# Kernel optimization log

Hardware: AMD Instinct MI355X
Metric: run time of the kernel (lower is better)

Reference implementation:

```python
import jax, jax.numpy as jnp
import numpy as np

VOCAB = 100000
TOPK = 20
EMB = 300
BS, SEQ = 64, 256

def setup_inputs() -> dict:
    key = jax.random.key(0)
    k1, k2, k3, k4, k5 = jax.random.split(key, 5)
    conceptnet_text_vec = jax.random.randint(k1, (BS, SEQ), 0, VOCAB)
    neighbors = jax.random.randint(k2, (VOCAB, TOPK), 0, VOCAB)
    emb = jax.random.normal(k3, (VOCAB, EMB), dtype=jnp.float32)
    # xavier-normal init for attention params
    a = jax.random.normal(k4, (EMB, EMB), dtype=jnp.float32) * np.sqrt(2.0 / (EMB + EMB))
    b = jax.random.normal(k5, (EMB, 1), dtype=jnp.float32) * np.sqrt(2.0 / (EMB + 1))
    return {"conceptnet_text_vec": conceptnet_text_vec, "neighbors": neighbors,
            "emb": emb, "a": a, "b": b}

def reference(conceptnet_text_vec, neighbors, emb, a, b):
    # double gather: ids -> neighbor ids -> neighbor embeddings
    nb = neighbors[conceptnet_text_vec]          # [B, S, K] int
    h = emb[nb]                                  # [B, S, K, D]
    # tanh attention scores over the K (neighbor) dim
    e = jnp.einsum('bske,e->bsk', jnp.tanh(jnp.einsum('bskd,de->bske', h, a)), b[:, 0])
    att = jax.nn.softmax(e, axis=-1)             # [B, S, K]
    return jnp.einsum('bsk,bskd->bsd', att, h)   # [B, S, D]
```

## Files before the change

kernel.cpp:

```cpp
#include <hip/hip_runtime.h>
#include <hip/hip_bf16.h>
#include <math.h>

#define VOCAB 100000
#define TOPK  20
#define EMB   300
#define NTOK  (64*256)
#define NB    1563
#define NSLICE 128

typedef __attribute__((ext_vector_type(8))) short short8;
typedef __attribute__((ext_vector_type(4))) short short4v;
typedef __attribute__((ext_vector_type(4))) float f32x4;

static __device__ inline short f2bf(float f) {
    __hip_bfloat16 h = __float2bfloat16(f);
    short s; __builtin_memcpy(&s, &h, 2);
    return s;
}

__global__ void prep_kernel(const float* __restrict__ A, short* __restrict__ aT)
{
    const int e = blockIdx.x;
    for (int d = threadIdx.x; d < 320; d += 256) {
        float f = (e < EMB && d < EMB) ? A[(size_t)d * EMB + e] : 0.f;
        aT[e * 320 + d] = f2bf(f);
    }
}

__global__ __launch_bounds__(512, 2) void score_kernel(
    const float* __restrict__ emb, const short* __restrict__ aT,
    const float* __restrict__ B, float* __restrict__ S0, float* __restrict__ S1)
{
    __shared__ short8 BsS[160 * 40];
    __shared__ short8 EsS[64 * 40];
    __shared__ float  Sred[128];

    const int t     = threadIdx.x;
    const int eh    = blockIdx.x >> 7;
    const int slice = blockIdx.x & 127;

#pragma unroll
    for (int j = 0; j < 13; ++j) {
        const int i = t + j * 512;
        if (i < 6400) {
            const int col = i / 40, kc = i - col * 40;
            short8 v = ((const short8*)aT)[(eh * 160 + col) * 40 + kc];
            BsS[col * 40 + (kc ^ (col & 7))] = v;
        }
    }

    const int lid = t & 63;
    const int w   = t >> 6;
    const int kh  = w >> 2;
    const int mg  = (w >> 1) & 1;
    const int ng  = w & 1;
    const int lm  = lid & 15;
    const int lk  = lid >> 4;
    const int kh20  = kh * 20;
    const int xmask = lm & 7;

    int colb[5], rb[2];
    float bcol[5];
#pragma unroll
    for (int g = 0; g < 5; ++g) {
        const int col = (ng * 5 + g) * 16 + lm;
        colb[g] = col * 40;
        const int e = eh * 160 + col;
        bcol[g] = (e < EMB) ? B[e] : 0.f;
    }
#pragma unroll
    for (int mt = 0; mt < 2; ++mt)
        rb[mt] = (mg * 32 + mt * 16 + lm) * 40;

    const int ntiles = (NB - slice + NSLICE - 1) / NSLICE;
    float4 pf[10];

    {
        const float4* esrc = (const float4*)(emb + (size_t)slice * 64 * EMB);
#pragma unroll
        for (int j = 0; j < 10; ++j) {
            const int p4 = t + j * 512;
            float4 f = make_float4(0.f, 0.f, 0.f, 0.f);
            if (p4 < 4800 && slice * 64 + p4 / 75 < VOCAB) f = esrc[p4];
            pf[j] = f;
        }
    }

    for (int tt = 0; tt < ntiles; ++tt) {
        const int tile = slice + tt * NSLICE;
        const int v0   = tile * 64;

#pragma unroll
        for (int j = 0; j < 10; ++j) {
            const int p4 = t + j * 512;
            if (p4 < 4800) {
                const int row = p4 / 75, c4 = p4 - row * 75;
                short4v h;
                h.x = f2bf(pf[j].x); h.y = f2bf(pf[j].y);
                h.z = f2bf(pf[j].z); h.w = f2bf(pf[j].w);
                short* base = (short*)&EsS[row * 40 + ((c4 >> 1) ^ (row & 7))];
                *(short4v*)(base + (c4 & 1) * 4) = h;
            }
        }
        if (t < 320) {
            const int row = t / 5, q = t - row * 5;
            const int cc = 37 + ((q + 1) >> 1), half = (q + 1) & 1;
            short* base = (short*)&EsS[row * 40 + (cc ^ (row & 7))];
            *(short4v*)(base + half * 4) = (short4v){0, 0, 0, 0};
        }

        if (tt + 1 < ntiles) {
            const int tn = tile + NSLICE;
            const float4* esrc = (const float4*)(emb + (size_t)tn * 64 * EMB);
#pragma unroll
            for (int j = 0; j < 10; ++j) {
                const int p4 = t + j * 512;
                float4 f = make_float4(0.f, 0.f, 0.f, 0.f);
                if (p4 < 4800 && tn * 64 + p4 / 75 < VOCAB) f = esrc[p4];
                pf[j] = f;
            }
        }
        __syncthreads();

        f32x4 acc[2][5];
#pragma unroll
        for (int mt = 0; mt < 2; ++mt)
#pragma unroll
            for (int g = 0; g < 5; ++g)
                acc[mt][g] = (f32x4){0.f, 0.f, 0.f, 0.f};

        short8 bfr[2][5], afr[2][2];
        {
            const int kx = (kh20 + lk) ^ xmask;
#pragma unroll
            for (int g = 0; g < 5; ++g) bfr[0][g] = BsS[colb[g] + kx];
#pragma unroll
            for (int mt = 0; mt < 2; ++mt) afr[0][mt] = EsS[rb[mt] + kx];
        }
#pragma unroll
        for (int ks = 0; ks < 5; ++ks) {
            const int cur = ks & 1, nx = cur ^ 1;
            if (ks < 4) {
                const int kx = (kh20 + (ks + 1) * 4 + lk) ^ xmask;
#pragma unroll
                for (int g = 0; g < 5; ++g) bfr[nx][g] = BsS[colb[g] + kx];
#pragma unroll
                for (int mt = 0; mt < 2; ++mt) afr[nx][mt] = EsS[rb[mt] + kx];
            }
#pragma unroll
            for (int mt = 0; mt < 2; ++mt)
#pragma unroll
                for (int g = 0; g < 5; ++g)
                    acc[mt][g] = __builtin_amdgcn_mfma_f32_16x16x32_bf16(
                                     afr[cur][mt], bfr[cur][g], acc[mt][g], 0, 0, 0);
        }
        __syncthreads();

        float* scratchF = (float*)EsS;
        const int cell = mg * 2 + ng;
        if (kh == 1) {
#pragma unroll
            for (int mt = 0; mt < 2; ++mt)
#pragma unroll
                for (int g = 0; g < 5; ++g)
#pragma unroll
                    for (int i = 0; i < 4; ++i) {
                        const int q = (mt * 5 + g) * 4 + i;
                        scratchF[(q * 4 + cell) * 64 + lid] = acc[mt][g][i];
                    }
        }
        __syncthreads();

        if (kh == 0) {
            float part[2][4];
#pragma unroll
            for (int mt = 0; mt < 2; ++mt)
#pragma unroll
                for (int i = 0; i < 4; ++i) {
                    float p = 0.f;
#pragma unroll
                    for (int g = 0; g < 5; ++g) {
                        const int q = (mt * 5 + g) * 4 + i;
                        float x  = acc[mt][g][i] + scratchF[(q * 4 + cell) * 64 + lid];
                        float xc = fminf(fmaxf(x, -15.f), 15.f);
                        float e2 = __expf(2.f * xc);
                        p += __fdividef(e2 - 1.f, e2 + 1.f) * bcol[g];
                    }
                    part[mt][i] = p;
                }
#pragma unroll
            for (int m = 1; m <= 8; m <<= 1)
#pragma unroll
                for (int mt = 0; mt < 2; ++mt)
#pragma unroll
                    for (int i = 0; i < 4; ++i)
                        part[mt][i] += __shfl_xor(part[mt][i], m);
            if (lm == 0) {
#pragma unroll
                for (int mt = 0; mt < 2; ++mt)
#pragma unroll
                    for (int i = 0; i < 4; ++i)
                        Sred[ng * 64 + mg * 32 + mt * 16 + lk * 4 + i] = part[mt][i];
            }
        }
        __syncthreads();

        if (t < 64) {
            const int v = v0 + t;
            if (v < VOCAB) {
                float* Sp = eh ? S1 : S0;
                Sp[v] = Sred[t] + Sred[64 + t];
            }
        }
    }
}

__global__ __launch_bounds__(256) void attend_kernel(
    const int* __restrict__ text, const int* __restrict__ neighbors,
    const float* __restrict__ emb, const float* __restrict__ S0,
    const float* __restrict__ S1, float* __restrict__ out)
{
    const int lane = threadIdx.x & 63;
    const int wv   = threadIdx.x >> 6;
    const int tok  = blockIdx.x * 4 + wv;

    const int tid = text[tok];

    int   nbk = 0;
    float sc  = -1e30f;
    if (lane < TOPK) {
        nbk = neighbors[tid * TOPK + lane];
        sc  = S0[nbk] + S1[nbk];
    }

    float mx = sc;
#pragma unroll
    for (int m = 16; m >= 1; m >>= 1)
        mx = fmaxf(mx, __shfl_xor(mx, m));

    float ex = (lane < TOPK) ? expf(sc - mx) : 0.f;
    float sum = ex;
#pragma unroll
    for (int m = 16; m >= 1; m >>= 1)
        sum += __shfl_xor(sum, m);
    float att = ex / sum;

    float acc0 = 0.f, acc1 = 0.f, acc2 = 0.f, acc3 = 0.f, acc4 = 0.f;
    const bool has5 = (lane < EMB - 256);
#pragma unroll 4
    for (int k = 0; k < TOPK; ++k) {
        const float wgt = __shfl(att, k);
        const int   id  = __shfl(nbk, k);
        const float* row = emb + (size_t)id * EMB;
        acc0 = fmaf(wgt, row[lane      ], acc0);
        acc1 = fmaf(wgt, row[lane +  64], acc1);
        acc2 = fmaf(wgt, row[lane + 128], acc2);
        acc3 = fmaf(wgt, row[lane + 192], acc3);
        if (has5) acc4 = fmaf(wgt, row[lane + 256], acc4);
    }

    float* orow = out + (size_t)tok * EMB;
    orow[lane      ] = acc0;
    orow[lane +  64] = acc1;
    orow[lane + 128] = acc2;
    orow[lane + 192] = acc3;
    if (has5) orow[lane + 256] = acc4;
}

extern "C" void kernel_launch(void* const* d_in, const int* in_sizes, int n_in,
                              void* d_out, int out_size, void* d_ws, size_t ws_size,
                              hipStream_t stream) {
    const int*   text      = (const int*)d_in[0];
    const int*   neighbors = (const int*)d_in[1];
    const float* emb       = (const float*)d_in[2];
    const float* A         = (const float*)d_in[3];
    const float* B         = (const float*)d_in[4];
    float*       out       = (float*)d_out;

    char* ws = (char*)d_ws;
    float* S0 = (float*)ws;
    float* S1 = (float*)(ws + 400000);
    short* aT = (short*)(ws + 800000);

    prep_kernel<<<320, 256, 0, stream>>>(A, aT);
    score_kernel<<<256, 512, 0, stream>>>(emb, aT, B, S0, S1);
    attend_kernel<<<NTOK / 4, 256, 0, stream>>>(text, neighbors, emb, S0, S1, out);
}
```

Before: 129.0 us.

## Hold A-matrix fragments in registers and split tanh epilogue across both K-halves

The score kernel now loads each wave's bf16 A-transpose fragments straight into registers once, so the shared-memory B tile and its per-k-step LDS reads go away. The split-K reduction is rebalanced: each K-half writes the partial of the other's M-tile into a dedicated float4 scratch buffer, and both halves run the tanh/score epilogue, where before only one half did. Staging of the next embedding tile is moved into the reduction phase, and the emb loads use 8-element chunks with a separate tail load. This increases register pressure (25 short8 fragments held per thread) under the existing 512x2 launch bound, which could cause spills.

```diff
diff --git a/kernel.cpp b/kernel.cpp
--- a/kernel.cpp
+++ b/kernel.cpp
@@ -32,23 +32,13 @@
     const float* __restrict__ emb, const short* __restrict__ aT,
     const float* __restrict__ B, float* __restrict__ S0, float* __restrict__ S1)
 {
-    __shared__ short8 BsS[160 * 40];
     __shared__ short8 EsS[64 * 40];
+    __shared__ float4 Scr[2 * 5 * 4 * 64];
     __shared__ float  Sred[128];
 
     const int t     = threadIdx.x;
     const int eh    = blockIdx.x >> 7;
     const int slice = blockIdx.x & 127;
-
-#pragma unroll
-    for (int j = 0; j < 13; ++j) {
-        const int i = t + j * 512;
-        if (i < 6400) {
-            const int col = i / 40, kc = i - col * 40;
-            short8 v = ((const short8*)aT)[(eh * 160 + col) * 40 + kc];
-            BsS[col * 40 + (kc ^ (col & 7))] = v;
-        }
-    }
 
     const int lid = t & 63;
     const int w   = t >> 6;
@@ -57,152 +47,170 @@
     const int ng  = w & 1;
     const int lm  = lid & 15;
     const int lk  = lid >> 4;
-    const int kh20  = kh * 20;
+    const int kb    = kh * 20;
     const int xmask = lm & 7;
-
-    int colb[5], rb[2];
+    const int cell  = mg * 2 + ng;
+
+    const short8* aT8 = (const short8*)aT;
+    short8 bAll[5][5];
+#pragma unroll
+    for (int g = 0; g < 5; ++g) {
+        const int e = eh * 160 + ng * 80 + g * 16 + lm;
+#pragma unroll
+        for (int ks = 0; ks < 5; ++ks)
+            bAll[g][ks] = aT8[e * 40 + kb + ks * 4 + lk];
+    }
+
     float bcol[5];
 #pragma unroll
     for (int g = 0; g < 5; ++g) {
-        const int col = (ng * 5 + g) * 16 + lm;
-        colb[g] = col * 40;
-        const int e = eh * 160 + col;
+        const int e = eh * 160 + ng * 80 + g * 16 + lm;
         bcol[g] = (e < EMB) ? B[e] : 0.f;
     }
+    int rb[2];
 #pragma unroll
     for (int mt = 0; mt < 2; ++mt)
         rb[mt] = (mg * 32 + mt * 16 + lm) * 40;
 
     const int ntiles = (NB - slice + NSLICE - 1) / NSLICE;
-    float4 pf[10];
-
-    {
-        const float4* esrc = (const float4*)(emb + (size_t)slice * 64 * EMB);
-#pragma unroll
-        for (int j = 0; j < 10; ++j) {
-            const int p4 = t + j * 512;
-            float4 f = make_float4(0.f, 0.f, 0.f, 0.f);
-            if (p4 < 4800 && slice * 64 + p4 / 75 < VOCAB) f = esrc[p4];
-            pf[j] = f;
-        }
-    }
+
+    float4 pf[5][2]; float4 pft;
+    const int i0 = t, i1 = t + 512, i2 = t + 1024, i3 = t + 1536, i4 = t + 2048;
+
+#define ISSUE_PF(tn) do {                                                     \
+    const float4* esrc = (const float4*)(emb + (size_t)(tn) * 64 * EMB);      \
+    _Pragma("unroll")                                                         \
+    for (int j = 0; j < 5; ++j) {                                             \
+        const int i = t + j * 512;                                            \
+        const int row = i / 37, cc = i - row * 37;                            \
+        const bool ok = (i < 2368) && ((tn) * 64 + row < VOCAB);              \
+        pf[j][0] = ok ? esrc[row * 75 + cc * 2]     : make_float4(0,0,0,0);   \
+        pf[j][1] = ok ? esrc[row * 75 + cc * 2 + 1] : make_float4(0,0,0,0);   \
+    }                                                                         \
+    if (t < 64) pft = ((tn) * 64 + t < VOCAB) ? esrc[t * 75 + 74]             \
+                                              : make_float4(0,0,0,0);         \
+} while (0)
+
+#define STAGE() do {                                                          \
+    _Pragma("unroll")                                                         \
+    for (int j = 0; j < 5; ++j) {                                             \
+        const int i = t + j * 512;                                            \
+        if (i < 2368) {                                                       \
+            const int row = i / 37, cc = i - row * 37;                        \
+            short8 val;                                                       \
+            val[0]=f2bf(pf[j][0].x); val[1]=f2bf(pf[j][0].y);                 \
+            val[2]=f2bf(pf[j][0].z); val[3]=f2bf(pf[j][0].w);                 \
+            val[4]=f2bf(pf[j][1].x); val[5]=f2bf(pf[j][1].y);                 \
+            val[6]=f2bf(pf[j][1].z); val[7]=f2bf(pf[j][1].w);                 \
+            EsS[row * 40 + (cc ^ (row & 7))] = val;                           \
+        }                                                                     \
+    }                                                                         \
+    if (t < 64) {                                                             \
+        short4v h; h.x=f2bf(pft.x); h.y=f2bf(pft.y);                          \
+        h.z=f2bf(pft.z); h.w=f2bf(pft.w);                                     \
+        short* base = (short*)&EsS[t * 40 + (37 ^ (t & 7))];                  \
+        *(short4v*)(base) = h;                                                \
+        *(short4v*)(base + 4) = (short4v){0,0,0,0};                           \
+    }                                                                         \
+    if (t < 128) {                                                            \
+        const int row = t >> 1, cc = 38 + (t & 1);                            \
+        EsS[row * 40 + (cc ^ (row & 7))] = (short8){0,0,0,0,0,0,0,0};         \
+    }                                                                         \
+} while (0)
+
+    ISSUE_PF(slice);
+    STAGE();
+    ISSUE_PF(slice + NSLICE);
+    __syncthreads();
 
     for (int tt = 0; tt < ntiles; ++tt) {
         const int tile = slice + tt * NSLICE;
         const int v0   = tile * 64;
 
-#pragma unroll
-        for (int j = 0; j < 10; ++j) {
-            const int p4 = t + j * 512;
-            if (p4 < 4800) {
-                const int row = p4 / 75, c4 = p4 - row * 75;
-                short4v h;
-                h.x = f2bf(pf[j].x); h.y = f2bf(pf[j].y);
-                h.z = f2bf(pf[j].z); h.w = f2bf(pf[j].w);
-                short* base = (short*)&EsS[row * 40 + ((c4 >> 1) ^ (row & 7))];
-                *(short4v*)(base + (c4 & 1) * 4) = h;
-            }
-        }
-        if (t < 320) {
-            const int row = t / 5, q = t - row * 5;
-            const int cc = 37 + ((q + 1) >> 1), half = (q + 1) & 1;
-            short* base = (short*)&EsS[row * 40 + (cc ^ (row & 7))];
-            *(short4v*)(base + half * 4) = (short4v){0, 0, 0, 0};
-        }
-
-        if (tt + 1 < ntiles) {
-            const int tn = tile + NSLICE;
-            const float4* esrc = (const float4*)(emb + (size_t)tn * 64 * EMB);
-#pragma unroll
-            for (int j = 0; j < 10; ++j) {
-                const int p4 = t + j * 512;
-                float4 f = make_float4(0.f, 0.f, 0.f, 0.f);
-                if (p4 < 4800 && tn * 64 + p4 / 75 < VOCAB) f = esrc[p4];
-                pf[j] = f;
-            }
-        }
-        __syncthreads();
-
-        f32x4 acc[2][5];
-#pragma unroll
-        for (int mt = 0; mt < 2; ++mt)
-#pragma unroll
-            for (int g = 0; g < 5; ++g)
-                acc[mt][g] = (f32x4){0.f, 0.f, 0.f, 0.f};
-
-        short8 bfr[2][5], afr[2][2];
+        f32x4 acc0[5], acc1[5];
+#pragma unroll
+        for (int g = 0; g < 5; ++g) {
+            acc0[g] = (f32x4){0.f, 0.f, 0.f, 0.f};
+            acc1[g] = (f32x4){0.f, 0.f, 0.f, 0.f};
+        }
+        short8 afr[2][2];
         {
-            const int kx = (kh20 + lk) ^ xmask;
-#pragma unroll
-            for (int g = 0; g < 5; ++g) bfr[0][g] = BsS[colb[g] + kx];
-#pragma unroll
-            for (int mt = 0; mt < 2; ++mt) afr[0][mt] = EsS[rb[mt] + kx];
+            const int kx = (kb + lk) ^ xmask;
+            afr[0][0] = EsS[rb[0] + kx];
+            afr[0][1] = EsS[rb[1] + kx];
         }
 #pragma unroll
         for (int ks = 0; ks < 5; ++ks) {
             const int cur = ks & 1, nx = cur ^ 1;
             if (ks < 4) {
-                const int kx = (kh20 + (ks + 1) * 4 + lk) ^ xmask;
-#pragma unroll
-                for (int g = 0; g < 5; ++g) bfr[nx][g] = BsS[colb[g] + kx];
-#pragma unroll
-                for (int mt = 0; mt < 2; ++mt) afr[nx][mt] = EsS[rb[mt] + kx];
-            }
-#pragma unroll
-            for (int mt = 0; mt < 2; ++mt)
-#pragma unroll
-                for (int g = 0; g < 5; ++g)
-                    acc[mt][g] = __builtin_amdgcn_mfma_f32_16x16x32_bf16(
-                                     afr[cur][mt], bfr[cur][g], acc[mt][g], 0, 0, 0);
+                const int kx = (kb + (ks + 1) * 4 + lk) ^ xmask;
+                afr[nx][0] = EsS[rb[0] + kx];
+                afr[nx][1] = EsS[rb[1] + kx];
+            }
+#pragma unroll
+            for (int g = 0; g < 5; ++g) {
+                acc0[g] = __builtin_amdgcn_mfma_f32_16x16x32_bf16(
+                              afr[cur][0], bAll[g][ks], acc0[g], 0, 0, 0);
+                acc1[g] = __builtin_amdgcn_mfma_f32_16x16x32_bf16(
+                              afr[cur][1], bAll[g][ks], acc1[g], 0, 0, 0);
+            }
         }
         __syncthreads();
 
-        float* scratchF = (float*)EsS;
-        const int cell = mg * 2 + ng;
-        if (kh == 1) {
-#pragma unroll
-            for (int mt = 0; mt < 2; ++mt)
-#pragma unroll
-                for (int g = 0; g < 5; ++g)
-#pragma unroll
-                    for (int i = 0; i < 4; ++i) {
-                        const int q = (mt * 5 + g) * 4 + i;
-                        scratchF[(q * 4 + cell) * 64 + lid] = acc[mt][g][i];
-                    }
+        if (kh == 0) {
+#pragma unroll
+            for (int g = 0; g < 5; ++g)
+                Scr[((0 * 5 + g) * 4 + cell) * 64 + lid] = *(float4*)&acc1[g];
+        } else {
+#pragma unroll
+            for (int g = 0; g < 5; ++g)
+                Scr[((1 * 5 + g) * 4 + cell) * 64 + lid] = *(float4*)&acc0[g];
+        }
+        if (tt + 1 < ntiles) {
+            STAGE();
+            ISSUE_PF(slice + (tt + 2) * NSLICE);
         }
         __syncthreads();
 
+        float part[4];
         if (kh == 0) {
-            float part[2][4];
-#pragma unroll
-            for (int mt = 0; mt < 2; ++mt)
-#pragma unroll
-                for (int i = 0; i < 4; ++i) {
-                    float p = 0.f;
-#pragma unroll
-                    for (int g = 0; g < 5; ++g) {
-                        const int q = (mt * 5 + g) * 4 + i;
-                        float x  = acc[mt][g][i] + scratchF[(q * 4 + cell) * 64 + lid];
-                        float xc = fminf(fmaxf(x, -15.f), 15.f);
-                        float e2 = __expf(2.f * xc);
-                        p += __fdividef(e2 - 1.f, e2 + 1.f) * bcol[g];
-                    }
-                    part[mt][i] = p;
+#pragma unroll
+            for (int i = 0; i < 4; ++i) {
+                float p = 0.f;
+#pragma unroll
+                for (int g = 0; g < 5; ++g) {
+                    float4 o = Scr[((1 * 5 + g) * 4 + cell) * 64 + lid];
+                    float x  = acc0[g][i] + ((const float*)&o)[i];
+                    float xc = fminf(fmaxf(x, -15.f), 15.f);
+                    float e2 = __expf(2.f * xc);
+                    p += __fdividef(e2 - 1.f, e2 + 1.f) * bcol[g];
                 }
-#pragma unroll
-            for (int m = 1; m <= 8; m <<= 1)
-#pragma unroll
-                for (int mt = 0; mt < 2; ++mt)
-#pragma unroll
-                    for (int i = 0; i < 4; ++i)
-                        part[mt][i] += __shfl_xor(part[mt][i], m);
-            if (lm == 0) {
-#pragma unroll
-                for (int mt = 0; mt < 2; ++mt)
-#pragma unroll
-                    for (int i = 0; i < 4; ++i)
-                        Sred[ng * 64 + mg * 32 + mt * 16 + lk * 4 + i] = part[mt][i];
-            }
+                part[i] = p;
+            }
+        } else {
+#pragma unroll
+            for (int i = 0; i < 4; ++i) {
+                float p = 0.f;
+#pragma unroll
+                for (int g = 0; g < 5; ++g) {
+                    float4 o = Scr[((0 * 5 + g) * 4 + cell) * 64 + lid];
+                    float x  = acc1[g][i] + ((const float*)&o)[i];
+                    float xc = fminf(fmaxf(x, -15.f), 15.f);
+                    float e2 = __expf(2.f * xc);
+                    p += __fdividef(e2 - 1.f, e2 + 1.f) * bcol[g];
+                }
+                part[i] = p;
+            }
+        }
+#pragma unroll
+        for (int m = 1; m <= 8; m <<= 1)
+#pragma unroll
+            for (int i = 0; i < 4; ++i)
+                part[i] += __shfl_xor(part[i], m);
+        if (lm == 0) {
+#pragma unroll
+            for (int i = 0; i < 4; ++i)
+                Sred[ng * 64 + mg * 32 + kh * 16 + lk * 4 + i] = part[i];
         }
         __syncthreads();
 
@@ -214,6 +222,8 @@
             }
         }
     }
+#undef ISSUE_PF
+#undef STAGE
 }
 
 __global__ __launch_bounds__(256) void attend_kernel(
```

After: 143.1 us. 1.11x slower.
